# Kernel optimization log

Hardware: AMD Instinct MI355X
Metric: run time of the kernel (lower is better)

Reference implementation:

```python
import jax, jax.numpy as jnp
import numpy as np

N_HEADS = 16
N_QUBITS = 7
DIM = 2 ** N_QUBITS  # per-head state dimension = 128


def _rotation_gates(params):
    """params: [H, nq, 3] -> composite Rz@Ry@Rx gates [H, nq, 2, 2] complex64."""
    a = params[..., 0] / 2.0
    b = params[..., 1] / 2.0
    c = params[..., 2] / 2.0
    ca, sa = jnp.cos(a), jnp.sin(a)
    cb, sb = jnp.cos(b), jnp.sin(b)
    i_ = jnp.complex64(1j)
    rx = jnp.stack([jnp.stack([ca + 0j, -i_ * sa], -1),
                    jnp.stack([-i_ * sa, ca + 0j], -1)], -2)  # [H,nq,2,2]
    ry = jnp.stack([jnp.stack([cb + 0j, -sb + 0j], -1),
                    jnp.stack([sb + 0j, cb + 0j], -1)], -2)
    z = jnp.zeros_like(c) + 0j
    rz = jnp.stack([jnp.stack([jnp.exp(-i_ * c), z], -1),
                    jnp.stack([z, jnp.exp(i_ * c)], -1)], -2)
    return jnp.einsum('...ij,...jk,...kl->...il', rz, ry, rx).astype(jnp.complex64)


def _quantum_transform(states, params):
    """states: [B,S,H,D] real; params: [H,nq,3]. Apply per-qubit gates then measure |psi|^2.
    Qubit q acts on axis q of the state reshaped to [2]*n_qubits (q=0 most significant)."""
    B, S, H, D = states.shape
    gates = _rotation_gates(params)  # [H, nq, 2, 2]
    psi = states.astype(jnp.complex64)
    for q in range(N_QUBITS):
        L = 2 ** q
        R = D // (2 * L)
        psi = psi.reshape(B, S, H, L, 2, R)
        psi = jnp.einsum('hij,bshljr->bshlir', gates[:, q], psi)
        psi = psi.reshape(B, S, H, D)
    return psi.real ** 2 + psi.imag ** 2  # measurement probabilities, real fp32


def setup_inputs() -> dict:
    key = jax.random.key(0)
    ks = jax.random.split(key, 6)
    B, S = 2, 2048
    return {
        'states': jax.random.normal(ks[0], (B, S, N_HEADS * DIM), dtype=jnp.float32),
        'attention_mask': jnp.ones((B, S), dtype=jnp.int32),
        'query_params': jax.random.normal(ks[1], (N_HEADS, N_QUBITS, 3), dtype=jnp.float32),
        'key_params': jax.random.normal(ks[2], (N_HEADS, N_QUBITS, 3), dtype=jnp.float32),
        'value_params': jax.random.normal(ks[3], (N_HEADS, N_QUBITS, 3), dtype=jnp.float32),
        'W_out': jax.random.normal(ks[4], (DIM, N_HEADS * DIM), dtype=jnp.float32) / np.sqrt(N_HEADS * DIM),
        'b_out': jnp.zeros((DIM,), dtype=jnp.float32),
    }


def reference(states, attention_mask, query_params, key_params, value_params, W_out, b_out):
    B, S, F = states.shape
    x = states.reshape(B, S, N_HEADS, DIM)  # split heads
    q = _quantum_transform(x, query_params)   # [B,S,H,D]
    k = _quantum_transform(x, key_params)
    v = _quantum_transform(x, value_params)
    scores = jnp.einsum('bqhd,bkhd->bhqk', q, k) / np.sqrt(DIM)  # [B,H,S,S]
    mask = attention_mask[:, None, None, :] != 0  # [B,1,1,S]
    scores = jnp.where(mask, scores, jnp.float32(-jnp.inf))
    probs = jax.nn.softmax(scores, axis=-1)
    ctx = jnp.einsum('bhqk,bkhd->bqhd', probs, v)  # [B,S,H,D]
    concat = ctx.reshape(B, S, N_HEADS * DIM)
    return concat @ W_out.T + b_out  # [B,S,D]
```

## Files before the change

kernel.cpp:

```cpp
#include <hip/hip_runtime.h>
#include <math.h>

#define NH 16
#define DD 128
#define SS 2048
#define NQ 7

typedef __attribute__((ext_vector_type(8))) short bf16x8;
typedef __attribute__((ext_vector_type(16))) float f32x16;

#define MFMA32(a,b,c) __builtin_amdgcn_mfma_f32_32x32x16_bf16(a,b,c,0,0,0)

__device__ __forceinline__ unsigned pkbf(float a, float b){
    unsigned ua = __float_as_uint(a); ua += 0x7FFF + ((ua>>16)&1);
    unsigned ub = __float_as_uint(b); ub += 0x7FFF + ((ub>>16)&1);
    return (ua>>16) | (ub & 0xFFFF0000u);
}

__device__ __forceinline__ float fexp2(float x){
#if __has_builtin(__builtin_amdgcn_exp2f)
    return __builtin_amdgcn_exp2f(x);
#else
    return __expf(x * 0.69314718056f);
#endif
}

__device__ __forceinline__ void gl_lds16(const int4* g, int4* l){
    __builtin_amdgcn_global_load_lds((const __attribute__((address_space(1))) void*)g,
                                     (__attribute__((address_space(3))) void*)l, 16, 0, 0);
}

struct cplx { float r, i; };
__device__ __forceinline__ cplx cmul(cplx a, cplx b){ cplx o; o.r = a.r*b.r - a.i*b.i; o.i = a.r*b.i + a.i*b.r; return o; }
__device__ __forceinline__ cplx cadd(cplx a, cplx b){ cplx o; o.r = a.r+b.r; o.i = a.i+b.i; return o; }

__global__ void gates_kernel(const float* __restrict__ qp, const float* __restrict__ kp,
                             const float* __restrict__ vp, float* __restrict__ gates){
    for (int it = threadIdx.x; it < 3*NH*NQ; it += 256){
        int set = it / (NH*NQ);
        int rem = it % (NH*NQ);
        const float* p = (set==0 ? qp : (set==1 ? kp : vp)) + rem*3;
        float a = p[0]*0.5f, b = p[1]*0.5f, c = p[2]*0.5f;
        float ca=cosf(a), sa=sinf(a), cb=cosf(b), sb=sinf(b), cc=cosf(c), sc=sinf(c);
        cplx rx00={ca,0.f}, rx01={0.f,-sa}, rx10={0.f,-sa}, rx11={ca,0.f};
        cplx ry00={cb,0.f}, ry01={-sb,0.f}, ry10={sb,0.f}, ry11={cb,0.f};
        cplx e0={cc,-sc}, e1={cc,sc};
        cplx m00 = cadd(cmul(ry00,rx00), cmul(ry01,rx10));
        cplx m01 = cadd(cmul(ry00,rx01), cmul(ry01,rx11));
        cplx m10 = cadd(cmul(ry10,rx00), cmul(ry11,rx10));
        cplx m11 = cadd(cmul(ry10,rx01), cmul(ry11,rx11));
        cplx g00 = cmul(e0,m00), g01 = cmul(e0,m01), g10 = cmul(e1,m10), g11 = cmul(e1,m11);
        float* gp = gates + it*8;
        gp[0]=g00.r; gp[1]=g00.i; gp[2]=g01.r; gp[3]=g01.i;
        gp[4]=g10.r; gp[5]=g10.i; gp[6]=g11.r; gp[7]=g11.i;
    }
}

__global__ __launch_bounds__(256) void prep2_kernel(const float* __restrict__ W,
        const float* __restrict__ gates, ushort* __restrict__ wfrag, ushort* __restrict__ ufrag){
    int t = threadIdx.x;
    if (blockIdx.x < 128){
        int tid = blockIdx.x*256 + t;
        int ln = tid & 31, hi = (tid>>5)&1, ds = (tid>>6)&127, ct = tid>>13;
        int n = ct*32 + ln;
        const float* src = W + (size_t)n*2048 + ds*16 + hi*8;
        float4 f0 = *(const float4*)(src);
        float4 f1 = *(const float4*)(src + 4);
        int4 o;
        o.x = (int)pkbf(f0.x, f0.y); o.y = (int)pkbf(f0.z, f0.w);
        o.z = (int)pkbf(f1.x, f1.y); o.w = (int)pkbf(f1.z, f1.w);
        ((int4*)wfrag)[tid] = o;
        return;
    }
    int sh = blockIdx.x - 128;
    const float* gp = gates + sh*NQ*8;
    float g[7][8];
    #pragma unroll
    for (int q=0;q<7;++q)
        #pragma unroll
        for (int e=0;e<8;++e) g[q][e] = gp[q*8+e];
    int4* uf = (int4*)ufrag;
    #pragma unroll
    for (int p=0;p<8;++p){
        int pos = t + p*256;
        int ln = pos & 31, hi = (pos>>5)&1, ds = (pos>>6)&7, ct = pos>>9;
        int dp = ct*32 + ln;
        int d0 = ds*16 + hi*8;
        cplx base = {1.f, 0.f};
        #pragma unroll
        for (int q=0;q<4;++q){
            int rb = (dp >> (6-q)) & 1, cb2 = (d0 >> (6-q)) & 1;
            cplx gv = { g[q][rb*4+cb2*2], g[q][rb*4+cb2*2+1] };
            base = cmul(base, gv);
        }
        int r4 = (dp>>2)&1, r5 = (dp>>1)&1, r6 = dp&1;
        float vr[8], vi[8];
        #pragma unroll
        for (int j=0;j<8;++j){
            cplx g4 = { g[4][r4*4 + ((j>>2)&1)*2], g[4][r4*4 + ((j>>2)&1)*2 + 1] };
            cplx g5 = { g[5][r5*4 + ((j>>1)&1)*2], g[5][r5*4 + ((j>>1)&1)*2 + 1] };
            cplx g6 = { g[6][r6*4 + (j&1)*2],      g[6][r6*4 + (j&1)*2 + 1] };
            cplx v = cmul(cmul(cmul(base, g4), g5), g6);
            vr[j] = v.r; vi[j] = v.i;
        }
        int4 outr, outi;
        outr.x = (int)pkbf(vr[0],vr[1]); outr.y = (int)pkbf(vr[2],vr[3]);
        outr.z = (int)pkbf(vr[4],vr[5]); outr.w = (int)pkbf(vr[6],vr[7]);
        outi.x = (int)pkbf(vi[0],vi[1]); outi.y = (int)pkbf(vi[2],vi[3]);
        outi.z = (int)pkbf(vi[4],vi[5]); outi.w = (int)pkbf(vi[6],vi[7]);
        uf[ ((sh*8 + ct)*8 + ds)*64 + hi*32 + ln ]     = outr;
        uf[ ((sh*8 + 4 + ct)*8 + ds)*64 + hi*32 + ln ] = outi;
    }
}

__global__ __launch_bounds__(256, 2) void qkv_kernel(const float* __restrict__ states,
        const ushort* __restrict__ ufrag, ushort* __restrict__ qfo,
        ushort* __restrict__ kfo, ushort* __restrict__ vfo){
    __shared__ int xs[128*66];
    int t = threadIdx.x, w = t>>6, lane = t&63, hi = lane>>5, ln = lane&31;
    int blk = blockIdx.x;
    int set = blk >> 9;
    int r9  = blk & 511;
    int bh = r9 >> 4, stile = r9 & 15;
    int b = bh >> 4, h = bh & 15;
    const float sc = 0.12751743f;
    {
        int c = t & 31, tk2 = t >> 5;
        #pragma unroll
        for (int i=0;i<16;++i){
            int tk = i*8 + tk2;
            const float* src = states + ((size_t)(b*SS + stile*128 + tk))*2048 + h*128 + c*4;
            float4 f = *(const float4*)src;
            int2 o; o.x = (int)pkbf(f.x,f.y); o.y = (int)pkbf(f.z,f.w);
            *(int2*)(xs + tk*66 + c*2) = o;
        }
    }
    __syncthreads();
    int ct = w;
    int sh = set*16 + h;
    const int4* ub = (const int4*)ufrag;
    int4* qf4 = (int4*)qfo; int4* kf4 = (int4*)kfo; int4* vf4 = (int4*)vfo;
    bf16x8 ur[8], ui[8];
    #pragma unroll
    for (int ds=0; ds<8; ++ds){
        ur[ds] = *(const bf16x8*)(ub + ((sh*8 + ct)*8 + ds)*64 + lane);
        ui[ds] = *(const bf16x8*)(ub + ((sh*8 + 4 + ct)*8 + ds)*64 + lane);
    }
    #pragma unroll 1
    for (int tt=0; tt<4; ++tt){
        bf16x8 xf[8];
        #pragma unroll
        for (int ds=0; ds<8; ++ds){
            union { bf16x8 v; int2 d[2]; } c;
            const int2* base = (const int2*)(xs + (tt*32 + ln)*66 + ds*8 + hi*4);
            c.d[0] = base[0]; c.d[1] = base[1];
            xf[ds] = c.v;
        }
        f32x16 Cr, Ci;
        #pragma unroll
        for (int r=0;r<16;++r){ Cr[r]=0.f; Ci[r]=0.f; }
        if (set < 2){
            #pragma unroll
            for (int ds=0; ds<8; ++ds){
                Cr = MFMA32(ur[ds], xf[ds], Cr);
                Ci = MFMA32(ui[ds], xf[ds], Ci);
            }
        } else {
            #pragma unroll
            for (int ds=0; ds<8; ++ds){
                Cr = MFMA32(xf[ds], ur[ds], Cr);
                Ci = MFMA32(xf[ds], ui[ds], Ci);
            }
        }
        float pv[16];
        #pragma unroll
        for (int r=0;r<16;++r) pv[r] = Cr[r]*Cr[r] + Ci[r]*Ci[r];
        if (set == 0){
            #pragma unroll
            for (int r=0;r<16;++r) pv[r] *= sc;
        }
        unsigned u2[4][2];
        #pragma unroll
        for (int g2=0; g2<4; ++g2){
            u2[g2][0] = pkbf(pv[g2*4+0], pv[g2*4+1]);
            u2[g2][1] = pkbf(pv[g2*4+2], pv[g2*4+3]);
        }
        int mt = stile*4 + tt;
        #pragma unroll
        for (int gg=0; gg<2; ++gg){
            int g2s = hi*2 + gg, g2p = g2s ^ 2;
            unsigned r0 = (unsigned)__shfl_xor((int)u2[g2p][0], 32);
            unsigned r1 = (unsigned)__shfl_xor((int)u2[g2p][1], 32);
            int4 frag;
            frag.x = (int)(hi ? r0 : u2[g2s][0]);
            frag.y = (int)(hi ? r1 : u2[g2s][1]);
            frag.z = (int)(hi ? u2[g2s][0] : r0);
            frag.w = (int)(hi ? u2[g2s][1] : r1);
            if (set == 0)
                qf4[((bh*64 + mt)*8 + ct*2 + hi)*64 + gg*32 + ln] = frag;
            else if (set == 1)
                kf4[((bh*64 + mt)*8 + ct*2 + hi)*64 + gg*32 + ln] = frag;
            else
                vf4[((bh*4 + ct)*128 + mt*2 + hi)*64 + gg*32 + ln] = frag;
        }
    }
}

__global__ __launch_bounds__(256, 2) void flash_kernel(const ushort* __restrict__ qfi,
        const ushort* __restrict__ kfi, const ushort* __restrict__ vfi,
        const int* __restrict__ mask, ushort* __restrict__ ctxf){
    __shared__ __align__(16) int4 kbuf[2][1024];
    __shared__ __align__(16) int4 vbuf[2][1024];
    int t = threadIdx.x, w = t>>6, lane = t&63, hi = lane>>5, ln = lane&31;
    int bid = blockIdx.x;
    int i2 = bid >> 3;
    int bh = (bid & 7)*4 + (i2 & 3);
    int qt = i2 >> 2;
    int b = bh >> 4;
    const float NEGC = -57.7078018f;
    const int4* qfp = (const int4*)qfi + (size_t)((bh*64 + qt*4 + w)*8)*64 + lane;
    bf16x8 qf[8];
    #pragma unroll
    for (int ds=0; ds<8; ++ds) qf[ds] = *(const bf16x8*)(qfp + ds*64);
    const int4* kg = (const int4*)kfi + (size_t)(bh*64*8)*64 + (w*4)*64 + lane;
    const int4* vg = (const int4*)vfi + ((size_t)(bh*4 + w)*128)*64 + lane;
    const int* mp = mask + b*SS;
    f32x16 O[4];
    #pragma unroll
    for (int d=0; d<4; ++d){
        #pragma unroll
        for (int r=0;r<16;++r) O[d][r] = 0.f;
    }
    float l0=0.f, l1=0.f, l2=0.f, l3=0.f;
    {
        int4* kd = &kbuf[0][(w*4)*64];
        int4* vd = &vbuf[0][(w*4)*64];
        #pragma unroll
        for (int i=0;i<4;++i) gl_lds16(kg + i*64, kd + i*64);
        #pragma unroll
        for (int i=0;i<4;++i) gl_lds16(vg + i*64, vd + i*64);
    }
    for (int kt=0; kt<32; ++kt){
        int p = kt & 1;
        int mk = mp[kt*64 + lane];
        __syncthreads();
        if (kt < 31){
            int4* kd = &kbuf[p^1][(w*4)*64];
            int4* vd = &vbuf[p^1][(w*4)*64];
            const int4* ks = kg + (size_t)(kt+1)*1024;
            const int4* vs = vg + (kt+1)*4*64;
            #pragma unroll
            for (int i=0;i<4;++i) gl_lds16(ks + i*64, kd + i*64);
            #pragma unroll
            for (int i=0;i<4;++i) gl_lds16(vs + i*64, vd + i*64);
        }
        const int4* kl = kbuf[p];
        const int4* vl = vbuf[p];
        f32x16 S0, S1;
        #pragma unroll
        for (int r=0;r<16;++r){ S0[r]=NEGC; S1[r]=NEGC; }
        #pragma unroll
        for (int ds=0; ds<8; ++ds){
            bf16x8 k0 = *(const bf16x8*)(kl + ds*64 + lane);
            bf16x8 k1 = *(const bf16x8*)(kl + (8+ds)*64 + lane);
            S0 = MFMA32(k0, qf[ds], S0);
            S1 = MFMA32(k1, qf[ds], S1);
        }
        if (__ballot(mk != 0) != ~0ull){
            #pragma unroll
            for (int r=0;r<16;++r){
                int row0 = ((r>>2)<<3) + (hi<<2) + (r&3);
                if (__shfl(mk, row0) == 0)      S0[r] = -1e30f;
                if (__shfl(mk, 32 + row0) == 0) S1[r] = -1e30f;
            }
        }
        #pragma unroll
        for (int r=0;r<16;++r){
            S0[r] = fexp2(S0[r]);
            S1[r] = fexp2(S1[r]);
        }
        #pragma unroll
        for (int r=0;r<16;r+=4){
            l0 += S0[r];   l1 += S0[r+1]; l2 += S0[r+2]; l3 += S0[r+3];
            l0 += S1[r];   l1 += S1[r+1]; l2 += S1[r+2]; l3 += S1[r+3];
        }
        #pragma unroll
        for (int m2=0; m2<2; ++m2){
            #pragma unroll
            for (int T=0; T<2; ++T){
                const f32x16& P = m2 ? S1 : S0;
                unsigned A0 = pkbf(P[8*T+0], P[8*T+1]);
                unsigned A1 = pkbf(P[8*T+2], P[8*T+3]);
                unsigned B0 = pkbf(P[8*T+4], P[8*T+5]);
                unsigned B1 = pkbf(P[8*T+6], P[8*T+7]);
                unsigned X0 = hi ? A0 : B0, X1 = hi ? A1 : B1;
                unsigned Y0 = (unsigned)__shfl_xor((int)X0, 32);
                unsigned Y1 = (unsigned)__shfl_xor((int)X1, 32);
                union { bf16x8 v; unsigned u[4]; } pf;
                pf.u[0] = hi ? Y0 : A0;
                pf.u[1] = hi ? Y1 : A1;
                pf.u[2] = hi ? B0 : Y0;
                pf.u[3] = hi ? B1 : Y1;
                int tt = m2*2 + T;
                #pragma unroll
                for (int db=0; db<4; ++db){
                    bf16x8 vf = *(const bf16x8*)(vl + (db*4 + tt)*64 + lane);
                    O[db] = MFMA32(vf, pf.v, O[db]);
                }
            }
        }
    }
    float l = (l0+l1) + (l2+l3);
    l += __shfl_xor(l, 32);
    float inv = 1.f / l;
    int h = bh & 15;
    int mt = b*64 + qt*4 + w;
    int4* cf = (int4*)ctxf;
    #pragma unroll
    for (int db=0; db<4; ++db){
        unsigned u[4][2];
        #pragma unroll
        for (int g2=0; g2<4; ++g2){
            u[g2][0] = pkbf(O[db][g2*4+0]*inv, O[db][g2*4+1]*inv);
            u[g2][1] = pkbf(O[db][g2*4+2]*inv, O[db][g2*4+3]*inv);
        }
        #pragma unroll
        for (int gg=0; gg<2; ++gg){
            int g2s = hi*2 + gg;
            int g2p = g2s ^ 2;
            unsigned r0 = (unsigned)__shfl_xor((int)u[g2p][0], 32);
            unsigned r1 = (unsigned)__shfl_xor((int)u[g2p][1], 32);
            int4 frag;
            frag.x = (int)(hi ? r0 : u[g2s][0]);
            frag.y = (int)(hi ? r1 : u[g2s][1]);
            frag.z = (int)(hi ? u[g2s][0] : r0);
            frag.w = (int)(hi ? u[g2s][1] : r1);
            int ds = h*8 + db*2 + hi;
            cf[ ((size_t)(mt*128 + ds)*2 + gg)*32 + ln ] = frag;
        }
    }
}

__global__ __launch_bounds__(128) void proj_kernel(const ushort* __restrict__ ctxf,
                                                   const ushort* __restrict__ wfrag,
                                                   const float* __restrict__ bo,
                                                   float* __restrict__ out){
    __shared__ float ls[16][64];
    int t = threadIdx.x, w = t >> 6, lane = t & 63;
    int hi = lane >> 5, ln = lane & 31;
    int mt = blockIdx.x >> 2, ct = blockIdx.x & 3;
    const int4* A = (const int4*)ctxf + (size_t)mt*8192 + (size_t)w*64*64 + lane;
    const int4* B = (const int4*)wfrag + (size_t)ct*8192 + (size_t)w*64*64 + lane;
    f32x16 acc;
    #pragma unroll
    for (int r=0;r<16;++r) acc[r] = 0.f;
    #pragma unroll 8
    for (int ds=0; ds<64; ++ds){
        bf16x8 a = *(const bf16x8*)(A + (size_t)ds*64);
        bf16x8 b = *(const bf16x8*)(B + (size_t)ds*64);
        acc = MFMA32(a, b, acc);
    }
    if (w == 1){
        #pragma unroll
        for (int r=0;r<16;++r) ls[r][lane] = acc[r];
    }
    __syncthreads();
    if (w == 0){
        float bias = bo[ct*32 + ln];
        float* op = out + (size_t)(mt*32)*128 + ct*32 + ln;
        #pragma unroll
        for (int r=0;r<16;++r){
            int row = (r&3) + 8*(r>>2) + 4*hi;
            op[(size_t)row*128] = acc[r] + ls[r][lane] + bias;
        }
    }
}

extern "C" void kernel_launch(void* const* d_in, const int* in_sizes, int n_in,
                              void* d_out, int out_size, void* d_ws, size_t ws_size,
                              hipStream_t stream){
    const float* states = (const float*)d_in[0];
    const int*   mask   = (const int*)d_in[1];
    const float* qp     = (const float*)d_in[2];
    const float* kp     = (const float*)d_in[3];
    const float* vp     = (const float*)d_in[4];
    const float* W      = (const float*)d_in[5];
    const float* bo     = (const float*)d_in[6];
    float* out = (float*)d_out;
    char* wsb = (char*)d_ws;
    float*  gates = (float*) wsb;
    ushort* wfrag = (ushort*)(wsb + 16384);
    ushort* ufrag = (ushort*)(wsb + 16384 + 524288);
    char*   big   = wsb + 16384 + 524288 + 3145728;
    ushort* qf    = (ushort*)(big);
    ushort* kf    = (ushort*)(big + 1u*16777216);
    ushort* vf    = (ushort*)(big + 2u*16777216);
    ushort* ctxf  = (ushort*)(big + 3u*16777216);
    hipLaunchKernelGGL(gates_kernel, dim3(1), dim3(256), 0, stream, qp, kp, vp, gates);
    hipLaunchKernelGGL(prep2_kernel, dim3(176), dim3(256), 0, stream, W, gates, wfrag, ufrag);
    hipLaunchKernelGGL(qkv_kernel, dim3(1536), dim3(256), 0, stream, states, ufrag, qf, kf, vf);
    hipLaunchKernelGGL(flash_kernel, dim3(512), dim3(256), 0, stream, qf, kf, vf, mask, ctxf);
    hipLaunchKernelGGL(proj_kernel, dim3(512), dim3(128), 0, stream, ctxf, wfrag, bo, out);
}
```

Baseline: 220.1 us.

## Fuse gate computation into prep kernel and widen qkv and proj parallelism

Gate matrix computation moves into the prep kernel's ufrag blocks, which removes one kernel launch and the workspace round trip. The qkv kernel now handles 64-token tiles instead of 128, doubling the grid to 3072 blocks so the load spreads more evenly across CUs. The projection kernel splits its K reduction across 4 waves instead of 2 and sums the partials through LDS. These changes trade per-block reuse and extra LDS reduction work for more parallelism and fewer launches.

```diff
diff --git a/kernel.cpp b/kernel.cpp
--- a/kernel.cpp
+++ b/kernel.cpp
@@ -34,30 +34,9 @@
 __device__ __forceinline__ cplx cmul(cplx a, cplx b){ cplx o; o.r = a.r*b.r - a.i*b.i; o.i = a.r*b.i + a.i*b.r; return o; }
 __device__ __forceinline__ cplx cadd(cplx a, cplx b){ cplx o; o.r = a.r+b.r; o.i = a.i+b.i; return o; }
 
-__global__ void gates_kernel(const float* __restrict__ qp, const float* __restrict__ kp,
-                             const float* __restrict__ vp, float* __restrict__ gates){
-    for (int it = threadIdx.x; it < 3*NH*NQ; it += 256){
-        int set = it / (NH*NQ);
-        int rem = it % (NH*NQ);
-        const float* p = (set==0 ? qp : (set==1 ? kp : vp)) + rem*3;
-        float a = p[0]*0.5f, b = p[1]*0.5f, c = p[2]*0.5f;
-        float ca=cosf(a), sa=sinf(a), cb=cosf(b), sb=sinf(b), cc=cosf(c), sc=sinf(c);
-        cplx rx00={ca,0.f}, rx01={0.f,-sa}, rx10={0.f,-sa}, rx11={ca,0.f};
-        cplx ry00={cb,0.f}, ry01={-sb,0.f}, ry10={sb,0.f}, ry11={cb,0.f};
-        cplx e0={cc,-sc}, e1={cc,sc};
-        cplx m00 = cadd(cmul(ry00,rx00), cmul(ry01,rx10));
-        cplx m01 = cadd(cmul(ry00,rx01), cmul(ry01,rx11));
-        cplx m10 = cadd(cmul(ry10,rx00), cmul(ry11,rx10));
-        cplx m11 = cadd(cmul(ry10,rx01), cmul(ry11,rx11));
-        cplx g00 = cmul(e0,m00), g01 = cmul(e0,m01), g10 = cmul(e1,m10), g11 = cmul(e1,m11);
-        float* gp = gates + it*8;
-        gp[0]=g00.r; gp[1]=g00.i; gp[2]=g01.r; gp[3]=g01.i;
-        gp[4]=g10.r; gp[5]=g10.i; gp[6]=g11.r; gp[7]=g11.i;
-    }
-}
-
-__global__ __launch_bounds__(256) void prep2_kernel(const float* __restrict__ W,
-        const float* __restrict__ gates, ushort* __restrict__ wfrag, ushort* __restrict__ ufrag){
+__global__ __launch_bounds__(256) void prep2_kernel(const float* __restrict__ qp,
+        const float* __restrict__ kp, const float* __restrict__ vp,
+        const float* __restrict__ W, ushort* __restrict__ wfrag, ushort* __restrict__ ufrag){
     int t = threadIdx.x;
     if (blockIdx.x < 128){
         int tid = blockIdx.x*256 + t;
@@ -73,12 +52,29 @@
         return;
     }
     int sh = blockIdx.x - 128;
-    const float* gp = gates + sh*NQ*8;
+    __shared__ float gs[7][8];
+    if (t < 7){
+        int set = sh >> 4, h = sh & 15;
+        const float* p = (set==0 ? qp : (set==1 ? kp : vp)) + (h*NQ + t)*3;
+        float a = p[0]*0.5f, b = p[1]*0.5f, c = p[2]*0.5f;
+        float ca=cosf(a), sa=sinf(a), cb=cosf(b), sb=sinf(b), cc=cosf(c), sc=sinf(c);
+        cplx rx00={ca,0.f}, rx01={0.f,-sa}, rx10={0.f,-sa}, rx11={ca,0.f};
+        cplx ry00={cb,0.f}, ry01={-sb,0.f}, ry10={sb,0.f}, ry11={cb,0.f};
+        cplx e0={cc,-sc}, e1={cc,sc};
+        cplx m00 = cadd(cmul(ry00,rx00), cmul(ry01,rx10));
+        cplx m01 = cadd(cmul(ry00,rx01), cmul(ry01,rx11));
+        cplx m10 = cadd(cmul(ry10,rx00), cmul(ry11,rx10));
+        cplx m11 = cadd(cmul(ry10,rx01), cmul(ry11,rx11));
+        cplx g00 = cmul(e0,m00), g01 = cmul(e0,m01), g10 = cmul(e1,m10), g11 = cmul(e1,m11);
+        gs[t][0]=g00.r; gs[t][1]=g00.i; gs[t][2]=g01.r; gs[t][3]=g01.i;
+        gs[t][4]=g10.r; gs[t][5]=g10.i; gs[t][6]=g11.r; gs[t][7]=g11.i;
+    }
+    __syncthreads();
     float g[7][8];
     #pragma unroll
     for (int q=0;q<7;++q)
         #pragma unroll
-        for (int e=0;e<8;++e) g[q][e] = gp[q*8+e];
+        for (int e=0;e<8;++e) g[q][e] = gs[q][e];
     int4* uf = (int4*)ufrag;
     #pragma unroll
     for (int p=0;p<8;++p){
@@ -116,20 +112,20 @@
 __global__ __launch_bounds__(256, 2) void qkv_kernel(const float* __restrict__ states,
         const ushort* __restrict__ ufrag, ushort* __restrict__ qfo,
         ushort* __restrict__ kfo, ushort* __restrict__ vfo){
-    __shared__ int xs[128*66];
+    __shared__ int xs[64*66];
     int t = threadIdx.x, w = t>>6, lane = t&63, hi = lane>>5, ln = lane&31;
     int blk = blockIdx.x;
-    int set = blk >> 9;
-    int r9  = blk & 511;
-    int bh = r9 >> 4, stile = r9 & 15;
+    int set = blk >> 10;
+    int r10 = blk & 1023;
+    int bh = r10 >> 5, stile = r10 & 31;
     int b = bh >> 4, h = bh & 15;
     const float sc = 0.12751743f;
     {
         int c = t & 31, tk2 = t >> 5;
         #pragma unroll
-        for (int i=0;i<16;++i){
+        for (int i=0;i<8;++i){
             int tk = i*8 + tk2;
-            const float* src = states + ((size_t)(b*SS + stile*128 + tk))*2048 + h*128 + c*4;
+            const float* src = states + ((size_t)(b*SS + stile*64 + tk))*2048 + h*128 + c*4;
             float4 f = *(const float4*)src;
             int2 o; o.x = (int)pkbf(f.x,f.y); o.y = (int)pkbf(f.z,f.w);
             *(int2*)(xs + tk*66 + c*2) = o;
@@ -147,7 +143,7 @@
         ui[ds] = *(const bf16x8*)(ub + ((sh*8 + 4 + ct)*8 + ds)*64 + lane);
     }
     #pragma unroll 1
-    for (int tt=0; tt<4; ++tt){
+    for (int tt=0; tt<2; ++tt){
         bf16x8 xf[8];
         #pragma unroll
         for (int ds=0; ds<8; ++ds){
@@ -185,7 +181,7 @@
             u2[g2][0] = pkbf(pv[g2*4+0], pv[g2*4+1]);
             u2[g2][1] = pkbf(pv[g2*4+2], pv[g2*4+3]);
         }
-        int mt = stile*4 + tt;
+        int mt = stile*2 + tt;
         #pragma unroll
         for (int gg=0; gg<2; ++gg){
             int g2s = hi*2 + gg, g2p = g2s ^ 2;
@@ -341,28 +337,28 @@
     }
 }
 
-__global__ __launch_bounds__(128) void proj_kernel(const ushort* __restrict__ ctxf,
+__global__ __launch_bounds__(256) void proj_kernel(const ushort* __restrict__ ctxf,
                                                    const ushort* __restrict__ wfrag,
                                                    const float* __restrict__ bo,
                                                    float* __restrict__ out){
-    __shared__ float ls[16][64];
+    __shared__ float ls[3][16][64];
     int t = threadIdx.x, w = t >> 6, lane = t & 63;
     int hi = lane >> 5, ln = lane & 31;
     int mt = blockIdx.x >> 2, ct = blockIdx.x & 3;
-    const int4* A = (const int4*)ctxf + (size_t)mt*8192 + (size_t)w*64*64 + lane;
-    const int4* B = (const int4*)wfrag + (size_t)ct*8192 + (size_t)w*64*64 + lane;
+    const int4* A = (const int4*)ctxf + (size_t)mt*8192 + (size_t)w*32*64 + lane;
+    const int4* B = (const int4*)wfrag + (size_t)ct*8192 + (size_t)w*32*64 + lane;
     f32x16 acc;
     #pragma unroll
     for (int r=0;r<16;++r) acc[r] = 0.f;
     #pragma unroll 8
-    for (int ds=0; ds<64; ++ds){
+    for (int ds=0; ds<32; ++ds){
         bf16x8 a = *(const bf16x8*)(A + (size_t)ds*64);
         bf16x8 b = *(const bf16x8*)(B + (size_t)ds*64);
         acc = MFMA32(a, b, acc);
     }
-    if (w == 1){
-        #pragma unroll
-        for (int r=0;r<16;++r) ls[r][lane] = acc[r];
+    if (w > 0){
+        #pragma unroll
+        for (int r=0;r<16;++r) ls[w-1][r][lane] = acc[r];
     }
     __syncthreads();
     if (w == 0){
@@ -371,7 +367,8 @@
         #pragma unroll
         for (int r=0;r<16;++r){
             int row = (r&3) + 8*(r>>2) + 4*hi;
-            op[(size_t)row*128] = acc[r] + ls[r][lane] + bias;
+            float s = acc[r] + ls[0][r][lane] + ls[1][r][lane] + ls[2][r][lane] + bias;
+            op[(size_t)row*128] = s;
         }
     }
 }
@@ -388,7 +385,6 @@
     const float* bo     = (const float*)d_in[6];
     float* out = (float*)d_out;
     char* wsb = (char*)d_ws;
-    float*  gates = (float*) wsb;
     ushort* wfrag = (ushort*)(wsb + 16384);
     ushort* ufrag = (ushort*)(wsb + 16384 + 524288);
     char*   big   = wsb + 16384 + 524288 + 3145728;
@@ -396,9 +392,8 @@
     ushort* kf    = (ushort*)(big + 1u*16777216);
     ushort* vf    = (ushort*)(big + 2u*16777216);
     ushort* ctxf  = (ushort*)(big + 3u*16777216);
-    hipLaunchKernelGGL(gates_kernel, dim3(1), dim3(256), 0, stream, qp, kp, vp, gates);
-    hipLaunchKernelGGL(prep2_kernel, dim3(176), dim3(256), 0, stream, W, gates, wfrag, ufrag);
-    hipLaunchKernelGGL(qkv_kernel, dim3(1536), dim3(256), 0, stream, states, ufrag, qf, kf, vf);
+    hipLaunchKernelGGL(prep2_kernel, dim3(176), dim3(256), 0, stream, qp, kp, vp, W, wfrag, ufrag);
+    hipLaunchKernelGGL(qkv_kernel, dim3(3072), dim3(256), 0, stream, states, ufrag, qf, kf, vf);
     hipLaunchKernelGGL(flash_kernel, dim3(512), dim3(256), 0, stream, qf, kf, vf, mask, ctxf);
-    hipLaunchKernelGGL(proj_kernel, dim3(512), dim3(128), 0, stream, ctxf, wfrag, bo, out);
-}
+    hipLaunchKernelGGL(proj_kernel, dim3(512), dim3(256), 0, stream, ctxf, wfrag, bo, out);
+}
```

After: 218.1 us. Within noise of the previous version (-0.9%).
